# Performance work log

Measured on AMD Instinct MI355X. Metric: run time of the kernel, lower is better.

Reference implementation:

```python
import jax, jax.numpy as jnp
import numpy as np

N = 100000          # nodes
E = 1600000         # edges
IN_DIM, HID, OUT = 64, 64, 32  # last GCN layer outputs OUT+1 channels


def setup_inputs() -> dict:
    key = jax.random.key(0)
    k0, k1, k2, k3 = jax.random.split(key, 4)
    x = jax.random.normal(k0, (N, IN_DIM), dtype=jnp.float32)
    edge_index = jax.random.randint(k1, (2, E), 0, N, dtype=jnp.int32)
    W1 = jax.random.normal(k2, (IN_DIM, HID), dtype=jnp.float32) / np.sqrt(IN_DIM)
    b1 = jnp.zeros((HID,), jnp.float32)
    W2 = jax.random.normal(k3, (HID, OUT + 1), dtype=jnp.float32) / np.sqrt(HID)
    b2 = jnp.zeros((OUT + 1,), jnp.float32)
    return {"x": x, "W1": W1, "b1": b1, "W2": W2, "b2": b2, "edge_index": edge_index}


def gcn_conv(x, src, dst, W, b):
    """PyG GCNConv: x' = D^{-1/2}(A+I)D^{-1/2} x W + b (self-loops added)."""
    n = x.shape[0]
    h = x @ W                                   # [N, F_out]
    # in-degree (over target nodes) + 1 for the self-loop
    deg = jnp.zeros((n,), x.dtype).at[dst].add(1.0) + 1.0
    dinv = jax.lax.rsqrt(deg)                   # [N]
    norm = dinv[src] * dinv[dst]                # [E]
    agg = jax.ops.segment_sum(h[src] * norm[:, None], dst, num_segments=n)
    agg = agg + h * (dinv * dinv)[:, None]      # self-loop contribution
    return agg + b


def reference(x, W1, b1, W2, b2, edge_index):
    src, dst = edge_index[0], edge_index[1]
    h = jax.nn.relu(gcn_conv(x, src, dst, W1, b1))
    # nn.Dropout(0.5) is identity in eval mode
    h = gcn_conv(h, src, dst, W2, b2)
    pos = h[:, :OUT]                            # [N, OUT]
    mass = jnp.exp(h[:, OUT:])                  # [N, 1]
    return pos, mass
```

## Files before the change

kernel.cpp:

```cpp
#include <hip/hip_runtime.h>
#include <hip/hip_bf16.h>


constexpr int NN = 100000;
constexpr int NE = 1600000;

constexpr int BSHIFT = 9;
constexpr int NBUCK = (NN + (1 << BSHIFT) - 1) >> BSHIFT;
constexpr int TILE = 4096;
constexpr int NTILE = (NE + TILE - 1) / TILE;
constexpr int GEMM1CH = (NN + 255) / 256;
constexpr int CAP = 16384;


__device__ inline float bflo(unsigned w) { union { unsigned u; float f; } c; c.u = w << 16; return c.f; }
__device__ inline float bfhi(unsigned w) { union { unsigned u; float f; } c; c.u = w & 0xffff0000u; return c.f; }
__device__ inline unsigned f2bf_bits(float f) {
    __hip_bfloat16 h = __float2bfloat16(f);
    unsigned short u; __builtin_memcpy(&u, &h, 2); return (unsigned)u;
}
__device__ inline unsigned pack2(float a, float b) { return f2bf_bits(a) | (f2bf_bits(b) << 16); }


__global__ void k_zero(int* __restrict__ g) {
    int t = threadIdx.x;
    if (t < NBUCK) g[t] = 0;
}


__global__ __launch_bounds__(256, 1) void k_split_gemm(const int* __restrict__ src,
                                                       const int* __restrict__ dst,
                                                       int* __restrict__ gcur,
                                                       unsigned* __restrict__ pairs,
                                                       const float* __restrict__ x,
                                                       const float* __restrict__ W1,
                                                       unsigned short* __restrict__ ht1) {
    __shared__ __align__(16) char smem[23552];
    int tid = threadIdx.x;

    if (blockIdx.x < NTILE) {
        int* lcnt = (int*)smem;
        int* lpre = lcnt + 256;
        int* gadj = lpre + 256;
        unsigned* buf = (unsigned*)(gadj + 200);
        unsigned char* bb = (unsigned char*)(buf + TILE);
        int base = blockIdx.x * TILE;

        lcnt[tid] = 0;
        __syncthreads();

        unsigned pk[16]; short bk[16]; short lp[16];
        #pragma unroll
        for (int k = 0; k < 16; ++k) {
            int e = base + k * 256 + tid;
            bk[k] = -1;
            if (e < NE) {
                int s = src[e], d = dst[e];
                int b = d >> BSHIFT;
                pk[k] = (unsigned)s | ((unsigned)(d & ((1 << BSHIFT) - 1)) << 17);
                bk[k] = (short)b;
                lp[k] = (short)atomicAdd(&lcnt[b], 1);
            }
        }
        __syncthreads();

        lpre[tid] = lcnt[tid];
        __syncthreads();
        for (int off = 1; off < 256; off <<= 1) {
            int v = (tid >= off) ? lpre[tid - off] : 0;
            __syncthreads();
            lpre[tid] += v;
            __syncthreads();
        }
        int total = lpre[255];

        if (tid < NBUCK) {
            int ex = lpre[tid] - lcnt[tid];
            gadj[tid] = tid * CAP + atomicAdd(&gcur[tid], lcnt[tid]) - ex;
        }
        __syncthreads();

        #pragma unroll
        for (int k = 0; k < 16; ++k) {
            if (bk[k] >= 0) {
                int b = bk[k];
                int i = (lpre[b] - lcnt[b]) + lp[k];
                buf[i] = pk[k];
                bb[i] = (unsigned char)b;
            }
        }
        __syncthreads();

        for (int i = tid; i < total; i += 256) {
            pairs[gadj[bb[i]] + i] = buf[i];
        }
    } else {
        float* w = (float*)smem;
        for (int t = tid; t < 64 * 64; t += 256) w[t] = W1[t];
        __syncthreads();

        int i = (blockIdx.x - NTILE) * 256 + tid;
        if (i >= NN) return;

        float acc[64];
        #pragma unroll
        for (int f = 0; f < 64; ++f) acc[f] = 0.f;

        const float4* xp = reinterpret_cast<const float4*>(x + (size_t)i * 64);
        #pragma unroll
        for (int kc = 0; kc < 4; ++kc) {
            float4 c0 = xp[4 * kc + 0], c1 = xp[4 * kc + 1];
            float4 c2 = xp[4 * kc + 2], c3 = xp[4 * kc + 3];
            float xs[16] = {c0.x, c0.y, c0.z, c0.w, c1.x, c1.y, c1.z, c1.w,
                            c2.x, c2.y, c2.z, c2.w, c3.x, c3.y, c3.z, c3.w};
            #pragma unroll
            for (int kk = 0; kk < 16; ++kk) {
                float xk = xs[kk];
                const float4* wr = reinterpret_cast<const float4*>(w + (16 * kc + kk) * 64);
                #pragma unroll
                for (int f4 = 0; f4 < 16; ++f4) {
                    float4 wv = wr[f4];
                    acc[4 * f4 + 0] += xk * wv.x;
                    acc[4 * f4 + 1] += xk * wv.y;
                    acc[4 * f4 + 2] += xk * wv.z;
                    acc[4 * f4 + 3] += xk * wv.w;
                }
            }
        }

        uint4* hp = reinterpret_cast<uint4*>(ht1 + (size_t)i * 64);
        #pragma unroll
        for (int q = 0; q < 8; ++q) {
            uint4 v;
            v.x = pack2(acc[8 * q + 0], acc[8 * q + 1]);
            v.y = pack2(acc[8 * q + 2], acc[8 * q + 3]);
            v.z = pack2(acc[8 * q + 4], acc[8 * q + 5]);
            v.w = pack2(acc[8 * q + 6], acc[8 * q + 7]);
            hp[q] = v;
        }
    }
}


__global__ __launch_bounds__(256) void k_bin2(const unsigned* __restrict__ pairs,
                                              const int* __restrict__ gcur,
                                              int* __restrict__ csr,
                                              int* __restrict__ rs,
                                              int* __restrict__ re,
                                              float* __restrict__ dinv) {
    int b = blockIdx.x;
    int lo = b << BSHIFT;
    int nn = min(1 << BSHIFT, NN - lo);
    int t = threadIdx.x;
    int beg = b * CAP;
    int endd = beg + gcur[b];

    __shared__ int lcnt[1 << BSHIFT];
    __shared__ int loff[1 << BSHIFT];
    __shared__ int wsum[256];

    for (int i = t; i < (1 << BSHIFT); i += 256) lcnt[i] = 0;
    __syncthreads();
    for (int idx = beg + t; idx < endd; idx += 256)
        atomicAdd(&lcnt[pairs[idx] >> 17], 1);
    __syncthreads();

    int v0 = lcnt[2 * t], v1 = lcnt[2 * t + 1];
    int s = v0 + v1;
    wsum[t] = s; __syncthreads();
    for (int off = 1; off < 256; off <<= 1) {
        int a = (t >= off) ? wsum[t - off] : 0;
        __syncthreads();
        wsum[t] += a;
        __syncthreads();
    }
    int ex = wsum[t] - s;
    loff[2 * t] = ex; loff[2 * t + 1] = ex + v0;
    __syncthreads();

    for (int i = t; i < nn; i += 256) {
        int st = beg + loff[i];
        rs[lo + i] = st;
        re[lo + i] = st + lcnt[i];
        dinv[lo + i] = rsqrtf((float)lcnt[i] + 1.0f);
    }
    __syncthreads();
    for (int i = t; i < (1 << BSHIFT); i += 256) lcnt[i] = 0;
    __syncthreads();

    for (int idx = beg + t; idx < endd; idx += 256) {
        unsigned v = pairs[idx];
        int dl = (int)(v >> 17);
        int p = atomicAdd(&lcnt[dl], 1);
        csr[beg + loff[dl] + p] = (int)(v & 0x1FFFFu);
    }
}


__global__ __launch_bounds__(256) void k_gather1(const unsigned short* __restrict__ ht,
                                                 const int* __restrict__ rs,
                                                 const int* __restrict__ re,
                                                 const int* __restrict__ csr,
                                                 const float* __restrict__ dinv,
                                                 const float* __restrict__ b1,
                                                 const float* __restrict__ W2,
                                                 unsigned short* __restrict__ htp,
                                                 float* __restrict__ htm) {
    __shared__ float w2s[64 * 36];
    __shared__ float hs[32 * 68];

    for (int t = threadIdx.x; t < 64 * 36; t += 256) {
        int k = t / 36, c = t - k * 36;
        w2s[t] = (c < 33) ? W2[k * 33 + c] : 0.f;
    }

    int wid = (blockIdx.x * 256 + threadIdx.x) >> 3;
    int g = threadIdx.x >> 3;
    int l = threadIdx.x & 7;
    int beg = rs[wid], end = re[wid];

    float av[8];
    #pragma unroll
    for (int k = 0; k < 8; ++k) av[k] = 0.f;

    for (int j0 = beg; j0 < end; j0 += 8) {
        int jj = j0 + l;
        int sv = csr[min(jj, end - 1)];
        float dvl = dinv[sv];
        uint4 rows[8]; float ds[8];
        #pragma unroll
        for (int e = 0; e < 8; ++e) {
            int s = __shfl(sv, e, 8);
            ds[e] = __shfl(dvl, e, 8);
            rows[e] = *reinterpret_cast<const uint4*>(ht + (size_t)s * 64 + 8 * l);
        }
        #pragma unroll
        for (int e = 0; e < 8; ++e) {
            float msk = (j0 + e < end) ? ds[e] : 0.f;
            uint4 w = rows[e];
            av[0] += msk * bflo(w.x); av[1] += msk * bfhi(w.x);
            av[2] += msk * bflo(w.y); av[3] += msk * bfhi(w.y);
            av[4] += msk * bflo(w.z); av[5] += msk * bfhi(w.z);
            av[6] += msk * bflo(w.w); av[7] += msk * bfhi(w.w);
        }
    }

    float di = dinv[wid];
    uint4 sw = *reinterpret_cast<const uint4*>(ht + (size_t)wid * 64 + 8 * l);
    av[0] += di * bflo(sw.x); av[1] += di * bfhi(sw.x);
    av[2] += di * bflo(sw.y); av[3] += di * bfhi(sw.y);
    av[4] += di * bflo(sw.z); av[5] += di * bfhi(sw.z);
    av[6] += di * bflo(sw.w); av[7] += di * bfhi(sw.w);

    const float4* bp = reinterpret_cast<const float4*>(b1 + 8 * l);
    float4 bA = bp[0], bB = bp[1];
    float4 vA, vB;
    vA.x = fmaxf(di * av[0] + bA.x, 0.f); vA.y = fmaxf(di * av[1] + bA.y, 0.f);
    vA.z = fmaxf(di * av[2] + bA.z, 0.f); vA.w = fmaxf(di * av[3] + bA.w, 0.f);
    vB.x = fmaxf(di * av[4] + bB.x, 0.f); vB.y = fmaxf(di * av[5] + bB.y, 0.f);
    vB.z = fmaxf(di * av[6] + bB.z, 0.f); vB.w = fmaxf(di * av[7] + bB.w, 0.f);
    float* hp = hs + g * 68 + 8 * l;
    *reinterpret_cast<float4*>(hp)     = vA;
    *reinterpret_cast<float4*>(hp + 4) = vB;
    __syncthreads();

    float acc0 = 0.f, acc1 = 0.f, acc2 = 0.f, acc3 = 0.f, accm = 0.f;
    const float* hrow = hs + g * 68;
    #pragma unroll 8
    for (int k = 0; k < 64; ++k) {
        float hv = hrow[k];
        const float* wr = w2s + k * 36 + 4 * l;
        acc0 += hv * wr[0];
        acc1 += hv * wr[1];
        acc2 += hv * wr[2];
        acc3 += hv * wr[3];
        accm += hv * w2s[k * 36 + 32];
    }
    uint2 pv;
    pv.x = pack2(acc0 * di, acc1 * di);
    pv.y = pack2(acc2 * di, acc3 * di);
    *reinterpret_cast<uint2*>(htp + (size_t)wid * 32 + 4 * l) = pv;
    if (l == 0) htm[wid] = accm * di;
}


__global__ __launch_bounds__(256) void k_gather2(const unsigned short* __restrict__ htp,
                                                 const float* __restrict__ htm,
                                                 const int* __restrict__ rs,
                                                 const int* __restrict__ re,
                                                 const int* __restrict__ csr,
                                                 const float* __restrict__ dinv,
                                                 const float* __restrict__ b2,
                                                 float* __restrict__ out) {
    int wid = (blockIdx.x * 256 + threadIdx.x) >> 3;
    int l = threadIdx.x & 7;
    int beg = rs[wid], end = re[wid];

    float a0 = 0.f, a1 = 0.f, a2 = 0.f, a3 = 0.f, m = 0.f;
    for (int j0 = beg; j0 < end; j0 += 8) {
        int jj = j0 + l;
        int sv = csr[min(jj, end - 1)];
        if (jj < end) m += htm[sv];
        uint2 rows[8];
        #pragma unroll
        for (int e = 0; e < 8; ++e) {
            int s = __shfl(sv, e, 8);
            rows[e] = *reinterpret_cast<const uint2*>(htp + (size_t)s * 32 + 4 * l);
        }
        #pragma unroll
        for (int e = 0; e < 8; ++e) {
            float msk = (j0 + e < end) ? 1.f : 0.f;
            uint2 w = rows[e];
            a0 += msk * bflo(w.x); a1 += msk * bfhi(w.x);
            a2 += msk * bflo(w.y); a3 += msk * bfhi(w.y);
        }
    }

    m += __shfl_xor(m, 1); m += __shfl_xor(m, 2); m += __shfl_xor(m, 4);

    float di = dinv[wid];
    uint2 sw = *reinterpret_cast<const uint2*>(htp + (size_t)wid * 32 + 4 * l);
    a0 += bflo(sw.x); a1 += bfhi(sw.x); a2 += bflo(sw.y); a3 += bfhi(sw.y);
    const float4* bp = reinterpret_cast<const float4*>(b2 + 4 * l);
    float4 bv = bp[0];
    float4 v;
    v.x = di * a0 + bv.x; v.y = di * a1 + bv.y;
    v.z = di * a2 + bv.z; v.w = di * a3 + bv.w;
    *reinterpret_cast<float4*>(out + (size_t)wid * 32 + 4 * l) = v;
    if (l == 0) {
        out[(size_t)NN * 32 + wid] = expf(di * (m + htm[wid]) + b2[32]);
    }
}

extern "C" void kernel_launch(void* const* d_in, const int* in_sizes, int n_in,
                              void* d_out, int out_size, void* d_ws, size_t ws_size,
                              hipStream_t stream) {
    const float* x  = (const float*)d_in[0];
    const float* W1 = (const float*)d_in[1];
    const float* b1 = (const float*)d_in[2];
    const float* W2 = (const float*)d_in[3];
    const float* b2 = (const float*)d_in[4];
    const int*   ei = (const int*)d_in[5];
    const int* src = ei;
    const int* dst = ei + NE;
    float* out = (float*)d_out;

    char* p = (char*)d_ws;
    int* gcur   = (int*)p;              p += sizeof(int) * NBUCK;
    p = (char*)(((uintptr_t)p + 255) & ~(uintptr_t)255);
    int* rs     = (int*)p;              p += sizeof(int) * NN;
    p = (char*)(((uintptr_t)p + 255) & ~(uintptr_t)255);
    int* re     = (int*)p;              p += sizeof(int) * NN;
    p = (char*)(((uintptr_t)p + 255) & ~(uintptr_t)255);
    int* csr    = (int*)p;              p += sizeof(int) * (size_t)NBUCK * CAP;
    p = (char*)(((uintptr_t)p + 255) & ~(uintptr_t)255);
    unsigned* pairs = (unsigned*)p;     p += sizeof(unsigned) * (size_t)NBUCK * CAP;
    p = (char*)(((uintptr_t)p + 255) & ~(uintptr_t)255);
    float* dinv = (float*)p;            p += sizeof(float) * NN;
    p = (char*)(((uintptr_t)p + 255) & ~(uintptr_t)255);
    unsigned short* ht1 = (unsigned short*)p; p += sizeof(unsigned short) * (size_t)NN * 64;
    p = (char*)(((uintptr_t)p + 255) & ~(uintptr_t)255);
    unsigned short* htp = (unsigned short*)p; p += sizeof(unsigned short) * (size_t)NN * 32;
    p = (char*)(((uintptr_t)p + 255) & ~(uintptr_t)255);
    float* htm  = (float*)p;            p += sizeof(float) * NN;

    k_zero<<<1, 256, 0, stream>>>(gcur);
    k_split_gemm<<<NTILE + GEMM1CH, 256, 0, stream>>>(src, dst, gcur, pairs, x, W1, ht1);
    k_bin2<<<NBUCK, 256, 0, stream>>>(pairs, gcur, csr, rs, re, dinv);

    k_gather1<<<(NN * 8) / 256, 256, 0, stream>>>(ht1, rs, re, csr, dinv, b1, W2, htp, htm);

    k_gather2<<<(NN * 8) / 256, 256, 0, stream>>>(htp, htm, rs, re, csr, dinv, b2, out);
}
```

Measured before the change: 145.9 us.

## Pre-scale layer-1 features by dinv in a separate pass, halve split tile

The first GEMM now writes fp32 x·W1 to a new workspace buffer, and a new k_scale kernel multiplies each row by its source-node dinv before packing it to bf16. This lets k_gather1 drop the per-edge dinv gather and shuffle. The edge-split tile size is halved, which doubles the number of split blocks and shrinks their shared memory. In exchange the pipeline gets an extra launch plus an extra 25.6MB fp32 write and read.

```diff
diff --git a/kernel.cpp b/kernel.cpp
--- a/kernel.cpp
+++ b/kernel.cpp
@@ -7,7 +7,7 @@
 
 constexpr int BSHIFT = 9;
 constexpr int NBUCK = (NN + (1 << BSHIFT) - 1) >> BSHIFT;
-constexpr int TILE = 4096;
+constexpr int TILE = 2048;
 constexpr int NTILE = (NE + TILE - 1) / TILE;
 constexpr int GEMM1CH = (NN + 255) / 256;
 constexpr int CAP = 16384;
@@ -34,8 +34,8 @@
                                                        unsigned* __restrict__ pairs,
                                                        const float* __restrict__ x,
                                                        const float* __restrict__ W1,
-                                                       unsigned short* __restrict__ ht1) {
-    __shared__ __align__(16) char smem[23552];
+                                                       float* __restrict__ xw) {
+    __shared__ __align__(16) char smem[16384];
     int tid = threadIdx.x;
 
     if (blockIdx.x < NTILE) {
@@ -49,9 +49,9 @@
         lcnt[tid] = 0;
         __syncthreads();
 
-        unsigned pk[16]; short bk[16]; short lp[16];
-        #pragma unroll
-        for (int k = 0; k < 16; ++k) {
+        unsigned pk[8]; short bk[8]; short lp[8];
+        #pragma unroll
+        for (int k = 0; k < 8; ++k) {
             int e = base + k * 256 + tid;
             bk[k] = -1;
             if (e < NE) {
@@ -81,7 +81,7 @@
         __syncthreads();
 
         #pragma unroll
-        for (int k = 0; k < 16; ++k) {
+        for (int k = 0; k < 8; ++k) {
             if (bk[k] >= 0) {
                 int b = bk[k];
                 int i = (lpre[b] - lcnt[b]) + lp[k];
@@ -128,14 +128,12 @@
             }
         }
 
-        uint4* hp = reinterpret_cast<uint4*>(ht1 + (size_t)i * 64);
-        #pragma unroll
-        for (int q = 0; q < 8; ++q) {
-            uint4 v;
-            v.x = pack2(acc[8 * q + 0], acc[8 * q + 1]);
-            v.y = pack2(acc[8 * q + 2], acc[8 * q + 3]);
-            v.z = pack2(acc[8 * q + 4], acc[8 * q + 5]);
-            v.w = pack2(acc[8 * q + 6], acc[8 * q + 7]);
+        float4* hp = reinterpret_cast<float4*>(xw + (size_t)i * 64);
+        #pragma unroll
+        for (int q = 0; q < 16; ++q) {
+            float4 v;
+            v.x = acc[4 * q + 0]; v.y = acc[4 * q + 1];
+            v.z = acc[4 * q + 2]; v.w = acc[4 * q + 3];
             hp[q] = v;
         }
     }
@@ -197,6 +195,23 @@
 }
 
 
+__global__ __launch_bounds__(256) void k_scale(const float* __restrict__ xw,
+                                               const float* __restrict__ dinv,
+                                               unsigned short* __restrict__ ht1) {
+    int t = blockIdx.x * 256 + threadIdx.x;
+    int i = t >> 3, seg = t & 7;
+    float di = dinv[i];
+    const float4* xp = reinterpret_cast<const float4*>(xw + (size_t)i * 64 + seg * 8);
+    float4 a = xp[0], b = xp[1];
+    uint4 v;
+    v.x = pack2(a.x * di, a.y * di);
+    v.y = pack2(a.z * di, a.w * di);
+    v.z = pack2(b.x * di, b.y * di);
+    v.w = pack2(b.z * di, b.w * di);
+    *reinterpret_cast<uint4*>(ht1 + (size_t)i * 64 + seg * 8) = v;
+}
+
+
 __global__ __launch_bounds__(256) void k_gather1(const unsigned short* __restrict__ ht,
                                                  const int* __restrict__ rs,
                                                  const int* __restrict__ re,
@@ -226,17 +241,15 @@
     for (int j0 = beg; j0 < end; j0 += 8) {
         int jj = j0 + l;
         int sv = csr[min(jj, end - 1)];
-        float dvl = dinv[sv];
-        uint4 rows[8]; float ds[8];
+        uint4 rows[8];
         #pragma unroll
         for (int e = 0; e < 8; ++e) {
             int s = __shfl(sv, e, 8);
-            ds[e] = __shfl(dvl, e, 8);
             rows[e] = *reinterpret_cast<const uint4*>(ht + (size_t)s * 64 + 8 * l);
         }
         #pragma unroll
         for (int e = 0; e < 8; ++e) {
-            float msk = (j0 + e < end) ? ds[e] : 0.f;
+            float msk = (j0 + e < end) ? 1.f : 0.f;
             uint4 w = rows[e];
             av[0] += msk * bflo(w.x); av[1] += msk * bfhi(w.x);
             av[2] += msk * bflo(w.y); av[3] += msk * bfhi(w.y);
@@ -245,13 +258,11 @@
         }
     }
 
+    uint4 sw = *reinterpret_cast<const uint4*>(ht + (size_t)wid * 64 + 8 * l);
+    av[0] += bflo(sw.x); av[1] += bfhi(sw.x); av[2] += bflo(sw.y); av[3] += bfhi(sw.y);
+    av[4] += bflo(sw.z); av[5] += bfhi(sw.z); av[6] += bflo(sw.w); av[7] += bfhi(sw.w);
+
     float di = dinv[wid];
-    uint4 sw = *reinterpret_cast<const uint4*>(ht + (size_t)wid * 64 + 8 * l);
-    av[0] += di * bflo(sw.x); av[1] += di * bfhi(sw.x);
-    av[2] += di * bflo(sw.y); av[3] += di * bfhi(sw.y);
-    av[4] += di * bflo(sw.z); av[5] += di * bfhi(sw.z);
-    av[6] += di * bflo(sw.w); av[7] += di * bfhi(sw.w);
-
     const float4* bp = reinterpret_cast<const float4*>(b1 + 8 * l);
     float4 bA = bp[0], bB = bp[1];
     float4 vA, vB;
@@ -358,6 +369,8 @@
     p = (char*)(((uintptr_t)p + 255) & ~(uintptr_t)255);
     float* dinv = (float*)p;            p += sizeof(float) * NN;
     p = (char*)(((uintptr_t)p + 255) & ~(uintptr_t)255);
+    float* xw   = (float*)p;            p += sizeof(float) * (size_t)NN * 64;
+    p = (char*)(((uintptr_t)p + 255) & ~(uintptr_t)255);
     unsigned short* ht1 = (unsigned short*)p; p += sizeof(unsigned short) * (size_t)NN * 64;
     p = (char*)(((uintptr_t)p + 255) & ~(uintptr_t)255);
     unsigned short* htp = (unsigned short*)p; p += sizeof(unsigned short) * (size_t)NN * 32;
@@ -365,8 +378,9 @@
     float* htm  = (float*)p;            p += sizeof(float) * NN;
 
     k_zero<<<1, 256, 0, stream>>>(gcur);
-    k_split_gemm<<<NTILE + GEMM1CH, 256, 0, stream>>>(src, dst, gcur, pairs, x, W1, ht1);
+    k_split_gemm<<<NTILE + GEMM1CH, 256, 0, stream>>>(src, dst, gcur, pairs, x, W1, xw);
     k_bin2<<<NBUCK, 256, 0, stream>>>(pairs, gcur, csr, rs, re, dinv);
+    k_scale<<<(NN * 8) / 256, 256, 0, stream>>>(xw, dinv, ht1);
 
     k_gather1<<<(NN * 8) / 256, 256, 0, stream>>>(ht1, rs, re, csr, dinv, b1, W2, htp, htm);
 
```

New measurement: 153.6 us. +5.2%, slower.
